# Optimization experiments

Hardware: AMD Instinct MI355X
Metric: run time of the kernel (lower is better)

The kernel has to match this reference:

```python
import jax, jax.numpy as jnp
import numpy as np

H, T, D = 16, 2048, 1024
DH = D // H  # 64


def setup_inputs() -> dict:
    key = jax.random.key(0)
    ks = jax.random.split(key, 6)
    state = jax.random.normal(ks[0], (H, DH, DH), jnp.float32) * 0.02  # per-head recurrent state
    x = jax.random.normal(ks[1], (T, D), jnp.float32)
    done = jax.random.uniform(ks[2], (T,)) < (4.0 / T)  # sparse episode-reset flags (bool)
    w_qkv = jax.random.normal(ks[3], (D, 3 * D), jnp.float32) / np.sqrt(D)
    b_qkv = jnp.zeros((3 * D,), jnp.float32)
    w_out = jax.random.normal(ks[4], (D, D), jnp.float32) / np.sqrt(D)
    b_out = jnp.zeros((D,), jnp.float32)
    return {"state": state, "x": x, "done": done, "w_qkv": w_qkv,
            "b_qkv": b_qkv, "w_out": w_out, "b_out": b_out}


def _mha_forward(state, x, done, w_qkv, b_qkv, w_out, b_out):
    # qkv projection; einops 'T (QKV H Dh) -> QKV H T Dh'
    qkv = (x @ w_qkv + b_qkv).reshape(T, 3, H, DH).transpose(1, 2, 0, 3)
    q, k, v = qkv[0], qkv[1], qkv[2]  # each (H, T, Dh)

    cum = jnp.cumsum(done.astype(jnp.int32))  # inclusive cumsum, as in done.cumsum()
    before_first = cum == 0            # tokens before first reset (attend to carried state)
    after_last = cum == cum[-1]        # tokens after last reset (feed new state)
    done_any = cum[-1] > 0

    # make_attn_mask(done): causal AND no reset index i with s < i <= t.
    # The scanned mask equals: causal & (cum[t] == cum[s]) (same-segment).
    t_idx = jnp.arange(T)
    mask = (t_idx[:, None] >= t_idx[None, :]) & (cum[:, None] == cum[None, :])  # (T, T)

    attn = jnp.where(mask[None], jnp.einsum('htd,hsd->hts', q, k), 0.0)  # mask * (q @ k.T)
    q_bef = q * before_first[None, :, None]
    out = jnp.einsum('hts,hsd->htd', attn, v) + jnp.einsum('htd,hde->hte', q_bef, state)

    k_aft = k * after_last[None, :, None]
    v_aft = v * after_last[None, :, None]
    s_new = jnp.einsum('htd,hte->hde', k_aft, v_aft)  # k_aft.T @ v_aft per head
    new_state = jnp.where(done_any, s_new, state + s_new)

    # 'H T Dh -> T (H Dh)' then output projection
    x_out = out.transpose(1, 0, 2).reshape(T, D) @ w_out + b_out
    return new_state, x_out


def reference(state, x, done, w_qkv, b_qkv, w_out, b_out):
    return _mha_forward(state, x, done, w_qkv, b_qkv, w_out, b_out)
```

## Files before the change

### kernel.cpp

```cpp
#include <hip/hip_runtime.h>

#define TT 2048
#define DD 1024
#define HH 16
#define DH 64
#define QKV_N 3072
#define QKW 2048

typedef __attribute__((ext_vector_type(8))) short bf16x8;
typedef __attribute__((ext_vector_type(4))) short short4v;
typedef __attribute__((ext_vector_type(4))) float f32x4;

__device__ inline short f2bf(float f) {
    union { float f; unsigned u; } v; v.f = f;
    unsigned r = v.u + 0x7fff + ((v.u >> 16) & 1);
    return (short)(r >> 16);
}

__device__ inline f32x4 mfma16(bf16x8 a, bf16x8 b, f32x4 c) {
    return __builtin_amdgcn_mfma_f32_16x16x32_bf16(a, b, c, 0, 0, 0);
}

__device__ __forceinline__ void gload16(const void* g, void* l) {
    __builtin_amdgcn_global_load_lds(
        (const __attribute__((address_space(1))) unsigned int*)g,
        (__attribute__((address_space(3))) unsigned int*)l, 16, 0, 0);
}

__device__ void transpose_tile(const float* __restrict__ in, short* __restrict__ out,
                               int R, int C, int r0, int c0, float (*tile)[65]) {
    int tid = threadIdx.x;
#pragma unroll
    for (int p = 0; p < 4; ++p) {
        int ch = tid + p * 256;
        int r = ch >> 4, c4 = (ch & 15) * 4;
        float4 v = *(const float4*)&in[(size_t)(r0 + r) * C + c0 + c4];
        tile[r][c4] = v.x; tile[r][c4 + 1] = v.y; tile[r][c4 + 2] = v.z; tile[r][c4 + 3] = v.w;
    }
    __syncthreads();
#pragma unroll
    for (int p = 0; p < 2; ++p) {
        int ch = tid + p * 256;
        int c = ch >> 3, r8 = (ch & 7) * 8;
        short tmp[8];
#pragma unroll
        for (int i = 0; i < 8; ++i) tmp[i] = f2bf(tile[r8 + i][c]);
        *(float4*)&out[(size_t)(c0 + c) * R + r0 + r8] = *(float4*)tmp;
    }
}

__global__ __launch_bounds__(256) void prep_kernel(const float* __restrict__ x,
                                                   const float* __restrict__ w_qkv,
                                                   const float* __restrict__ w_out,
                                                   const float* __restrict__ state,
                                                   const int* __restrict__ done,
                                                   const float* __restrict__ b_out,
                                                   short* __restrict__ x_bf,
                                                   short* __restrict__ wqT,
                                                   short* __restrict__ woT,
                                                   short* __restrict__ stT,
                                                   float* __restrict__ stout,
                                                   float* __restrict__ x_out,
                                                   int* __restrict__ seg,
                                                   int* __restrict__ totalp,
                                                   int* __restrict__ aux) {
    __shared__ float tile[64][65];
    __shared__ int scanbuf[2048 + 512 + 1];
    int b = blockIdx.x;
    int tid = threadIdx.x;
    if (b < 1024) {
        int i = (b * 256 + tid) * 8;
        float4 a = *(const float4*)&x[i];
        float4 c = *(const float4*)&x[i + 4];
        short tmp[8] = {f2bf(a.x), f2bf(a.y), f2bf(a.z), f2bf(a.w),
                        f2bf(c.x), f2bf(c.y), f2bf(c.z), f2bf(c.w)};
        *(float4*)&x_bf[i] = *(float4*)tmp;
    } else if (b < 1792) {
        int bb = b - 1024;
        transpose_tile(w_qkv, wqT, DD, QKV_N, (bb & 15) * 64, (bb >> 4) * 64, tile);
    } else if (b < 2048) {
        int bb = b - 1792;
        transpose_tile(w_out, woT, DD, DD, (bb & 15) * 64, (bb >> 4) * 64, tile);
    } else if (b < 2064) {
        int h = b - 2048;
        transpose_tile(state + (size_t)h * 4096, stT + (size_t)h * 4096, DH, DH, 0, 0, tile);
    } else if (b < 2128) {
        __shared__ int anyf;
        if (tid == 0) anyf = 0;
        __syncthreads();
        int acc = 0;
#pragma unroll
        for (int i = 0; i < 8; ++i) acc |= done[tid * 8 + i];
        if (acc) anyf = 1;
        __syncthreads();
        int f = ((b - 2064) * 256 + tid) * 4;
        float4 v = anyf ? make_float4(0.f, 0.f, 0.f, 0.f) : *(const float4*)&state[f];
        *(float4*)&stout[f] = v;
    } else if (b < 4176) {
        int f = ((b - 2128) * 256 + tid) * 4;
        int col = f & (DD - 1);
        *(float4*)&x_out[f] = *(const float4*)&b_out[col];
    } else {
        int* segl = scanbuf;
        int* part = scanbuf + 2048;
        int* excl = scanbuf + 2304;
        int base = tid * 8;
        int local[8];
        int run = 0;
#pragma unroll
        for (int i = 0; i < 8; ++i) { run += (done[base + i] != 0) ? 1 : 0; local[i] = run; }
        part[tid] = run;
        __syncthreads();
        if (tid < 64) {
            int p4[4];
#pragma unroll
            for (int i = 0; i < 4; ++i) p4[i] = part[tid * 4 + i];
            int s = p4[0] + p4[1] + p4[2] + p4[3];
            int v = s;
#pragma unroll
            for (int off = 1; off < 64; off <<= 1) {
                int u = __shfl_up(v, off);
                if (tid >= off) v += u;
            }
            int ex = v - s;
#pragma unroll
            for (int i = 0; i < 4; ++i) { excl[tid * 4 + i] = ex; ex += p4[i]; }
            if (tid == 63) { totalp[0] = v; scanbuf[2560] = v; }
        }
        __syncthreads();
        int off = excl[tid];
#pragma unroll
        for (int i = 0; i < 8; ++i) {
            int sv = off + local[i];
            seg[base + i] = sv;
            segl[base + i] = sv;
        }
        __syncthreads();
        if (tid < 33) {
            int target = (tid < 32) ? segl[tid * 64] : scanbuf[2560];
            int lo = 0, hi = 2047;
            while (lo < hi) { int mid = (lo + hi) >> 1; if (segl[mid] >= target) hi = mid; else lo = mid + 1; }
            aux[tid] = lo >> 6;
        }
    }
}

__global__ __launch_bounds__(256) void gemm_qkv(const short* __restrict__ A,
                                                const short* __restrict__ BT,
                                                const float* __restrict__ bias,
                                                short* __restrict__ qk,
                                                short* __restrict__ vt) {
    __shared__ __align__(16) short As[2][128 * 32];
    __shared__ __align__(16) short Bs[2][128 * 32];
    const int K = DD;
    int tid = threadIdx.x;
    int wave = tid >> 6, lane = tid & 63;
    int quad = lane >> 4, l15 = lane & 15;
    int m0 = blockIdx.x * 128, n0 = blockIdx.y * 128;
    int wr = (wave >> 1) * 64, wc = (wave & 1) * 64;

    int srow = wave * 32 + (lane >> 2);
    int scol = (lane & 3) * 8;
    const short* Ag = A + (size_t)(m0 + srow) * K + scol;
    const short* Bg = BT + (size_t)(n0 + srow) * K + scol;

    f32x4 acc[4][4] = {};
    for (int k0 = 0; k0 < K; k0 += 64) {
        __syncthreads();
#pragma unroll
        for (int g = 0; g < 2; ++g)
#pragma unroll
            for (int ks = 0; ks < 2; ++ks) {
                gload16(Ag + (size_t)g * 16 * K + k0 + ks * 32, &As[ks][(wave * 32 + g * 16) * 32]);
                gload16(Bg + (size_t)g * 16 * K + k0 + ks * 32, &Bs[ks][(wave * 32 + g * 16) * 32]);
            }
        __syncthreads();
#pragma unroll
        for (int ks = 0; ks < 2; ++ks) {
            bf16x8 af[4], bfr[4];
#pragma unroll
            for (int i = 0; i < 4; ++i) {
                af[i]  = *(const bf16x8*)&As[ks][(wr + i * 16 + l15) * 32 + quad * 8];
                bfr[i] = *(const bf16x8*)&Bs[ks][(wc + i * 16 + l15) * 32 + quad * 8];
            }
#pragma unroll
            for (int i = 0; i < 4; ++i)
#pragma unroll
                for (int j = 0; j < 4; ++j)
                    acc[i][j] = mfma16(af[i], bfr[j], acc[i][j]);
        }
    }

    if (n0 < 2048) {
#pragma unroll
        for (int i = 0; i < 4; ++i)
#pragma unroll
            for (int j = 0; j < 4; ++j)
#pragma unroll
                for (int r = 0; r < 4; ++r) {
                    int row = m0 + wr + i * 16 + quad * 4 + r;
                    int col = n0 + wc + j * 16 + l15;
                    qk[(size_t)row * QKW + col] = f2bf(acc[i][j][r] + bias[col]);
                }
    } else {
#pragma unroll
        for (int j = 0; j < 4; ++j) {
            int col = n0 + wc + j * 16 + l15;
            float bv = bias[col];
            int eg = col - 2048;
            int hh = eg >> 6, e = eg & 63;
#pragma unroll
            for (int i = 0; i < 4; ++i) {
                int tb = m0 + wr + i * 16 + quad * 4;
                short4v pk;
#pragma unroll
                for (int r = 0; r < 4; ++r) pk[r] = f2bf(acc[i][j][r] + bv);
                *(short4v*)&vt[(size_t)hh * (DH * TT) + (size_t)e * TT + tb] = pk;
            }
        }
    }
}

__global__ __launch_bounds__(256) void attn_mfma(const short* __restrict__ qk,
                                                 const short* __restrict__ vt,
                                                 const short* __restrict__ stT,
                                                 const int* __restrict__ seg,
                                                 const int* __restrict__ totalp,
                                                 const int* __restrict__ aux,
                                                 short* __restrict__ outb,
                                                 float* __restrict__ part,
                                                 float* __restrict__ nsout) {
    __shared__ __align__(16) short Qh[2][64 * 32];
    __shared__ __align__(16) short Kh[2][2][64 * 32];
    __shared__ __align__(16) short Vh[2][2][64 * 32];
    __shared__ __align__(16) short Ss[64 * 72];

    int h = blockIdx.x, tt = blockIdx.y, z = blockIdx.z;
    int t0 = tt * 64;
    int tid = threadIdx.x, wave = tid >> 6, lane = tid & 63;
    int quad = lane >> 4, l15 = lane & 15;
    int myt = wave * 16;
    const short* vbase = vt + (size_t)h * (DH * TT);

    if (z == 8) {
        if (tt < aux[32]) return;
        int total = totalp[0];
        int myd = wave * 16;
        short* K0 = Kh[0][0];
        short* K1 = Kh[0][1];
        bool keep = (seg[t0 + lane] == total);
        const short* src = qk + (size_t)(t0 + lane) * QKW + 1024 + h * DH + myd;
        union { float4 f; short s[8]; } u0, u1;
        u0.f = keep ? *(const float4*)src : make_float4(0.f, 0.f, 0.f, 0.f);
        u1.f = keep ? *(const float4*)(src + 8) : make_float4(0.f, 0.f, 0.f, 0.f);
        short* dst = (lane < 32) ? &K0[lane] : &K1[lane - 32];
#pragma unroll
        for (int i = 0; i < 8; ++i) {
            dst[(myd + i) * 32] = u0.s[i];
            dst[(myd + 8 + i) * 32] = u1.s[i];
        }
        bf16x8 a0 = *(const bf16x8*)&K0[(myd + l15) * 32 + quad * 8];
        bf16x8 a1 = *(const bf16x8*)&K1[(myd + l15) * 32 + quad * 8];
        f32x4 acc2[4] = {};
#pragma unroll
        for (int j = 0; j < 4; ++j) {
            const short* vrow = vbase + (size_t)(j * 16 + l15) * TT + t0 + quad * 8;
            bf16x8 b0 = *(const bf16x8*)vrow;
            bf16x8 b1 = *(const bf16x8*)(vrow + 32);
            acc2[j] = mfma16(a0, b0, acc2[j]);
            acc2[j] = mfma16(a1, b1, acc2[j]);
        }
        float* oh = nsout + (size_t)h * 4096;
#pragma unroll
        for (int j = 0; j < 4; ++j)
#pragma unroll
            for (int r = 0; r < 4; ++r)
                atomicAdd(&oh[(myd + quad * 4 + r) * DH + j * 16 + l15], acc2[j][r]);
        return;
    }

    int st0 = aux[tt];
    int sc_lo = st0 >> 2, sc_hi = tt >> 2;
    if (z < sc_lo || z > sc_hi) return;
    bool direct = (sc_lo == sc_hi);
    int st_lo = (st0 > z * 4) ? st0 : z * 4;
    int st_hi = (tt < z * 4 + 3) ? tt : z * 4 + 3;

    int sr = lane >> 2;
    int ch = lane & 3;
    const short* kg = qk + 1024 + h * DH;

    {
#pragma unroll
        for (int h2 = 0; h2 < 2; ++h2)
            gload16(qk + (size_t)(t0 + myt + sr) * QKW + h * DH + h2 * 32 + ch * 8,
                    &Qh[h2][myt * 32]);
        int s0 = st_lo * 64;
        gload16(kg + (size_t)(s0 + myt + sr) * QKW + ch * 8,      &Kh[0][0][myt * 32]);
        gload16(kg + (size_t)(s0 + myt + sr) * QKW + 32 + ch * 8, &Kh[0][1][myt * 32]);
        gload16(vbase + (size_t)(myt + sr) * TT + s0 + ch * 8,    &Vh[0][0][myt * 32]);
        gload16(vbase + (size_t)(myt + sr) * TT + s0 + 32 + ch * 8, &Vh[0][1][myt * 32]);
    }
    __syncthreads();

    bf16x8 af[2];
#pragma unroll
    for (int h2 = 0; h2 < 2; ++h2)
        af[h2] = *(const bf16x8*)&Qh[h2][(myt + l15) * 32 + quad * 8];

    int t_val = t0 + myt + l15;
    int seg_lane = seg[t_val];

    f32x4 acc2[4] = {};
    if (z == sc_lo && seg[t0] == 0) {
        const short* sb = stT + (size_t)h * 4096;
#pragma unroll
        for (int j = 0; j < 4; ++j)
#pragma unroll
            for (int h2 = 0; h2 < 2; ++h2) {
                bf16x8 a = *(const bf16x8*)(sb + (j * 16 + l15) * 64 + h2 * 32 + quad * 8);
                acc2[j] = mfma16(a, af[h2], acc2[j]);
            }
        if (seg_lane != 0) {
#pragma unroll
            for (int j = 0; j < 4; ++j)
#pragma unroll
                for (int r = 0; r < 4; ++r) acc2[j][r] = 0.f;
        }
    }

    int p = 0;
    for (int st = st_lo; st <= st_hi; ++st, p ^= 1) {
        if (st != st_lo) __syncthreads();
        if (st + 1 <= st_hi) {
            int s1 = (st + 1) * 64;
            gload16(kg + (size_t)(s1 + myt + sr) * QKW + ch * 8,        &Kh[p ^ 1][0][myt * 32]);
            gload16(kg + (size_t)(s1 + myt + sr) * QKW + 32 + ch * 8,   &Kh[p ^ 1][1][myt * 32]);
            gload16(vbase + (size_t)(myt + sr) * TT + s1 + ch * 8,      &Vh[p ^ 1][0][myt * 32]);
            gload16(vbase + (size_t)(myt + sr) * TT + s1 + 32 + ch * 8, &Vh[p ^ 1][1][myt * 32]);
        }
        int s0 = st * 64;

        f32x4 sacc[4] = {};
#pragma unroll
        for (int j = 0; j < 4; ++j)
#pragma unroll
            for (int h2 = 0; h2 < 2; ++h2) {
                bf16x8 kb = *(const bf16x8*)&Kh[p][h2][(j * 16 + l15) * 32 + quad * 8];
                sacc[j] = mfma16(kb, af[h2], sacc[j]);
            }
        int4 seg4[4];
#pragma unroll
        for (int j = 0; j < 4; ++j)
            seg4[j] = *(const int4*)&seg[s0 + j * 16 + quad * 4];
#pragma unroll
        for (int j = 0; j < 4; ++j) {
            short4v pk;
#pragma unroll
            for (int r = 0; r < 4; ++r) {
                int s_val = s0 + j * 16 + quad * 4 + r;
                int sv = (r == 0) ? seg4[j].x : (r == 1) ? seg4[j].y : (r == 2) ? seg4[j].z : seg4[j].w;
                bool ok = (sv == seg_lane) && (s_val <= t_val);
                pk[r] = ok ? f2bf(sacc[j][r]) : (short)0;
            }
            *(short4v*)&Ss[(myt + l15) * 72 + j * 16 + quad * 4] = pk;
        }
        bf16x8 sf[2];
#pragma unroll
        for (int h2 = 0; h2 < 2; ++h2)
            sf[h2] = *(const bf16x8*)&Ss[(myt + l15) * 72 + h2 * 32 + quad * 8];
#pragma unroll
        for (int j = 0; j < 4; ++j)
#pragma unroll
            for (int h2 = 0; h2 < 2; ++h2) {
                bf16x8 vb = *(const bf16x8*)&Vh[p][h2][(j * 16 + l15) * 32 + quad * 8];
                acc2[j] = mfma16(vb, sf[h2], acc2[j]);
            }
    }

    if (direct) {
#pragma unroll
        for (int j = 0; j < 4; ++j) {
            short4v pk;
#pragma unroll
            for (int r = 0; r < 4; ++r) pk[r] = f2bf(acc2[j][r]);
            *(short4v*)&outb[(size_t)t_val * DD + h * DH + j * 16 + quad * 4] = pk;
        }
    } else {
        float* pb = part + ((size_t)((h * 32 + tt) * 8 + z)) * 4096;
#pragma unroll
        for (int j = 0; j < 4; ++j)
            *(f32x4*)&pb[(myt + l15) * 64 + j * 16 + quad * 4] = acc2[j];
    }
}

__global__ __launch_bounds__(256) void attn_reduce(const float* __restrict__ part,
                                                   const int* __restrict__ aux,
                                                   short* __restrict__ outb) {
    int h = blockIdx.x, tt = blockIdx.y;
    int sc_lo = aux[tt] >> 2, sc_hi = tt >> 2;
    if (sc_lo == sc_hi) return;
    int t0 = tt * 64;
    int tid = threadIdx.x;
    const float* pb = part + ((size_t)(h * 32 + tt) * 8) * 4096;
#pragma unroll
    for (int p = 0; p < 4; ++p) {
        int idx = p * 256 + tid;
        int row = idx >> 4, c4 = (idx & 15) * 4;
        float4 acc = make_float4(0.f, 0.f, 0.f, 0.f);
        for (int sc = sc_lo; sc <= sc_hi; ++sc) {
            float4 v = *(const float4*)&pb[(size_t)sc * 4096 + row * 64 + c4];
            acc.x += v.x; acc.y += v.y; acc.z += v.z; acc.w += v.w;
        }
        short4v pk;
        pk[0] = f2bf(acc.x); pk[1] = f2bf(acc.y); pk[2] = f2bf(acc.z); pk[3] = f2bf(acc.w);
        *(short4v*)&outb[(size_t)(t0 + row) * DD + h * DH + c4] = pk;
    }
}

__global__ __launch_bounds__(256) void gemm_out(const short* __restrict__ A,
                                                const short* __restrict__ BT,
                                                float* __restrict__ Cout,
                                                int M, int N, int K) {
    __shared__ __align__(16) short As[128 * 32];
    __shared__ __align__(16) short Bs[128 * 32];
    int tid = threadIdx.x;
    int wave = tid >> 6, lane = tid & 63;
    int quad = lane >> 4, l15 = lane & 15;
    int m0 = blockIdx.x * 128, n0 = blockIdx.y * 128;
    int kb0 = blockIdx.z * (K / 2), kb1 = kb0 + K / 2;
    int wr = (wave >> 1) * 64, wc = (wave & 1) * 64;

    int srow = wave * 16 + (lane >> 2);
    int scol = (lane & 3) * 8;
    const short* Ag = A + (size_t)(m0 + srow) * K + scol;
    const short* Bg = BT + (size_t)(n0 + srow) * K + scol;
    short* As0 = &As[(wave * 16) * 32];
    short* As1 = &As[(64 + wave * 16) * 32];
    short* Bs0 = &Bs[(wave * 16) * 32];
    short* Bs1 = &Bs[(64 + wave * 16) * 32];

    f32x4 acc[4][4] = {};
    for (int k0 = kb0; k0 < kb1; k0 += 32) {
        __syncthreads();
        gload16(Ag + k0, As0);
        gload16(Ag + (size_t)64 * K + k0, As1);
        gload16(Bg + k0, Bs0);
        gload16(Bg + (size_t)64 * K + k0, Bs1);
        __syncthreads();
        bf16x8 af[4], bfr[4];
#pragma unroll
        for (int i = 0; i < 4; ++i) {
            af[i]  = *(const bf16x8*)&As[(wr + i * 16 + l15) * 32 + quad * 8];
            bfr[i] = *(const bf16x8*)&Bs[(wc + i * 16 + l15) * 32 + quad * 8];
        }
#pragma unroll
        for (int i = 0; i < 4; ++i)
#pragma unroll
            for (int j = 0; j < 4; ++j)
                acc[i][j] = mfma16(af[i], bfr[j], acc[i][j]);
    }
#pragma unroll
    for (int i = 0; i < 4; ++i)
#pragma unroll
        for (int j = 0; j < 4; ++j)
#pragma unroll
            for (int r = 0; r < 4; ++r) {
                int row = m0 + wr + i * 16 + quad * 4 + r;
                int col = n0 + wc + j * 16 + l15;
                atomicAdd(&Cout[(size_t)row * N + col], acc[i][j][r]);
            }
}

extern "C" void kernel_launch(void* const* d_in, const int* in_sizes, int n_in,
                              void* d_out, int out_size, void* d_ws, size_t ws_size,
                              hipStream_t stream) {
    const float* state = (const float*)d_in[0];
    const float* x     = (const float*)d_in[1];
    const int*   done  = (const int*)d_in[2];
    const float* w_qkv = (const float*)d_in[3];
    const float* b_qkv = (const float*)d_in[4];
    const float* w_out = (const float*)d_in[5];
    const float* b_out = (const float*)d_in[6];

    char* ws = (char*)d_ws;
    int*   seg    = (int*)ws;
    int*   totalp = (int*)(ws + 8192);
    int*   aux    = (int*)(ws + 8256);
    short* wqT    = (short*)(ws + 8448);
    short* woT    = (short*)(ws + 6299904);
    short* stT    = (short*)(ws + 8397056);
    short* qk     = (short*)(ws + 8528128);
    short* vt     = (short*)(ws + 16916736);
    short* xbf_outb = (short*)(ws + 21111040);
    float* part   = (float*)(ws + 25305344);

    float* new_state_out = (float*)d_out;
    float* x_out         = (float*)d_out + HH * DH * DH;

    prep_kernel<<<4177, 256, 0, stream>>>(x, w_qkv, w_out, state, done, b_out,
                                          xbf_outb, wqT, woT, stT,
                                          new_state_out, x_out, seg, totalp, aux);

    gemm_qkv<<<dim3(TT / 128, QKV_N / 128), 256, 0, stream>>>(
        xbf_outb, wqT, b_qkv, qk, vt);

    attn_mfma<<<dim3(HH, TT / 64, 9), 256, 0, stream>>>(
        qk, vt, stT, seg, totalp, aux, xbf_outb, part, new_state_out);

    attn_reduce<<<dim3(HH, TT / 64), 256, 0, stream>>>(part, aux, xbf_outb);

    gemm_out<<<dim3(TT / 128, DD / 128, 2), 256, 0, stream>>>(
        xbf_outb, woT, x_out, TT, DD, DD);
}
```

Baseline: 159.4 us.

## Fuse all stages into one persistent cooperative kernel with grid syncs

Replaces the five-kernel launch chain with a single cooperative persistent kernel of 512 blocks. Stages are separated by grid.sync, and the attention and state tasks are handed out through an atomic ticket queue. The QKV GEMM is retiled to 128x96 so each block owns one tile. The intent is to remove launch gaps and tail effects between stages. In exchange it adds grid-wide barrier cost and can lose occupancy or tile efficiency, and it keeps a multi-kernel fallback for when the cooperative launch fails.

New measurement: 473.0 us. 2.97x slower.

```diff
diff --git a/kernel.cpp b/kernel.cpp
--- a/kernel.cpp
+++ b/kernel.cpp
@@ -1,4 +1,5 @@
 #include <hip/hip_runtime.h>
+#include <hip/hip_cooperative_groups.h>
 
 #define TT 2048
 #define DD 1024
@@ -49,25 +50,13 @@
     }
 }
 
-__global__ __launch_bounds__(256) void prep_kernel(const float* __restrict__ x,
-                                                   const float* __restrict__ w_qkv,
-                                                   const float* __restrict__ w_out,
-                                                   const float* __restrict__ state,
-                                                   const int* __restrict__ done,
-                                                   const float* __restrict__ b_out,
-                                                   short* __restrict__ x_bf,
-                                                   short* __restrict__ wqT,
-                                                   short* __restrict__ woT,
-                                                   short* __restrict__ stT,
-                                                   float* __restrict__ stout,
-                                                   float* __restrict__ x_out,
-                                                   int* __restrict__ seg,
-                                                   int* __restrict__ totalp,
-                                                   int* __restrict__ aux) {
-    __shared__ float tile[64][65];
-    __shared__ int scanbuf[2048 + 512 + 1];
-    int b = blockIdx.x;
-    int tid = threadIdx.x;
+__device__ void prep_task(int b, int tid,
+                          const float* x, const float* w_qkv, const float* w_out,
+                          const float* state, const int* done, const float* b_out,
+                          short* x_bf, short* wqT, short* woT, short* stT,
+                          float* stout, float* x_out,
+                          int* seg, int* totalp, int* aux, int* ticket,
+                          float (*tile)[65], int* scanbuf) {
     if (b < 1024) {
         int i = (b * 256 + tid) * 8;
         float4 a = *(const float4*)&x[i];
@@ -85,14 +74,18 @@
         int h = b - 2048;
         transpose_tile(state + (size_t)h * 4096, stT + (size_t)h * 4096, DH, DH, 0, 0, tile);
     } else if (b < 2128) {
-        __shared__ int anyf;
-        if (tid == 0) anyf = 0;
-        __syncthreads();
         int acc = 0;
 #pragma unroll
         for (int i = 0; i < 8; ++i) acc |= done[tid * 8 + i];
-        if (acc) anyf = 1;
-        __syncthreads();
+        scanbuf[tid] = acc;
+        __syncthreads();
+        int any = 0;
+        for (int i = 0; i < 4; ++i) any |= scanbuf[((tid >> 2) * 4 + i) & 255];
+        any = __ballot(any != 0) != 0ull ? 1 : 0;
+        __syncthreads();
+        if (tid == 0) scanbuf[256] = any;
+        __syncthreads();
+        int anyf = scanbuf[256];
         int f = ((b - 2064) * 256 + tid) * 4;
         float4 v = anyf ? make_float4(0.f, 0.f, 0.f, 0.f) : *(const float4*)&state[f];
         *(float4*)&stout[f] = v;
@@ -102,19 +95,20 @@
         *(float4*)&x_out[f] = *(const float4*)&b_out[col];
     } else {
         int* segl = scanbuf;
-        int* part = scanbuf + 2048;
+        int* partb = scanbuf + 2048;
         int* excl = scanbuf + 2304;
         int base = tid * 8;
         int local[8];
         int run = 0;
 #pragma unroll
         for (int i = 0; i < 8; ++i) { run += (done[base + i] != 0) ? 1 : 0; local[i] = run; }
-        part[tid] = run;
+        partb[tid] = run;
+        if (tid == 0) *ticket = 0;
         __syncthreads();
         if (tid < 64) {
             int p4[4];
 #pragma unroll
-            for (int i = 0; i < 4; ++i) p4[i] = part[tid * 4 + i];
+            for (int i = 0; i < 4; ++i) p4[i] = partb[tid * 4 + i];
             int s = p4[0] + p4[1] + p4[2] + p4[3];
             int v = s;
 #pragma unroll
@@ -145,11 +139,381 @@
     }
 }
 
-__global__ __launch_bounds__(256) void gemm_qkv(const short* __restrict__ A,
-                                                const short* __restrict__ BT,
-                                                const float* __restrict__ bias,
-                                                short* __restrict__ qk,
-                                                short* __restrict__ vt) {
+__device__ void attn_task(int h, int tt, int z,
+                          const short* qk, const short* vt, const short* stT,
+                          const int* seg, const int* aux,
+                          short* outb, float* part,
+                          short* Qh0, short* Qh1, short* KhB, short* VhB, short* Ss,
+                          int tid, int wave, int lane, int quad, int l15) {
+    int st0 = aux[tt];
+    int sc_lo = st0 >> 2, sc_hi = tt >> 2;
+    if (z < sc_lo || z > sc_hi) return;
+    bool direct = (sc_lo == sc_hi);
+    int st_lo = (st0 > z * 4) ? st0 : z * 4;
+    int st_hi = (tt < z * 4 + 3) ? tt : z * 4 + 3;
+
+    int t0 = tt * 64;
+    int myt = wave * 16;
+    int sr = lane >> 2, ch = lane & 3;
+    const short* vbase = vt + (size_t)h * (DH * TT);
+    const short* kg = qk + 1024 + h * DH;
+
+    {
+        gload16(qk + (size_t)(t0 + myt + sr) * QKW + h * DH + ch * 8, Qh0 + myt * 32);
+        gload16(qk + (size_t)(t0 + myt + sr) * QKW + h * DH + 32 + ch * 8, Qh1 + myt * 32);
+        int s0 = st_lo * 64;
+        gload16(kg + (size_t)(s0 + myt + sr) * QKW + ch * 8,        KhB + 0 * 2048 + myt * 32);
+        gload16(kg + (size_t)(s0 + myt + sr) * QKW + 32 + ch * 8,   KhB + 1 * 2048 + myt * 32);
+        gload16(vbase + (size_t)(myt + sr) * TT + s0 + ch * 8,      VhB + 0 * 2048 + myt * 32);
+        gload16(vbase + (size_t)(myt + sr) * TT + s0 + 32 + ch * 8, VhB + 1 * 2048 + myt * 32);
+    }
+    __syncthreads();
+
+    bf16x8 af0 = *(const bf16x8*)&Qh0[(myt + l15) * 32 + quad * 8];
+    bf16x8 af1 = *(const bf16x8*)&Qh1[(myt + l15) * 32 + quad * 8];
+    int t_val = t0 + myt + l15;
+    int seg_lane = seg[t_val];
+
+    f32x4 acc2[4] = {};
+    if (z == sc_lo && seg[t0] == 0) {
+        const short* sb = stT + (size_t)h * 4096;
+#pragma unroll
+        for (int j = 0; j < 4; ++j) {
+            bf16x8 a0 = *(const bf16x8*)(sb + (j * 16 + l15) * 64 + quad * 8);
+            bf16x8 a1 = *(const bf16x8*)(sb + (j * 16 + l15) * 64 + 32 + quad * 8);
+            acc2[j] = mfma16(a0, af0, acc2[j]);
+            acc2[j] = mfma16(a1, af1, acc2[j]);
+        }
+        if (seg_lane != 0) {
+#pragma unroll
+            for (int j = 0; j < 4; ++j)
+#pragma unroll
+                for (int r = 0; r < 4; ++r) acc2[j][r] = 0.f;
+        }
+    }
+
+    int p = 0;
+    for (int st = st_lo; st <= st_hi; ++st, p ^= 1) {
+        if (st != st_lo) __syncthreads();
+        if (st + 1 <= st_hi) {
+            int s1 = (st + 1) * 64;
+            gload16(kg + (size_t)(s1 + myt + sr) * QKW + ch * 8,        KhB + ((p ^ 1) * 2 + 0) * 2048 + myt * 32);
+            gload16(kg + (size_t)(s1 + myt + sr) * QKW + 32 + ch * 8,   KhB + ((p ^ 1) * 2 + 1) * 2048 + myt * 32);
+            gload16(vbase + (size_t)(myt + sr) * TT + s1 + ch * 8,      VhB + ((p ^ 1) * 2 + 0) * 2048 + myt * 32);
+            gload16(vbase + (size_t)(myt + sr) * TT + s1 + 32 + ch * 8, VhB + ((p ^ 1) * 2 + 1) * 2048 + myt * 32);
+        }
+        int s0 = st * 64;
+
+        f32x4 sacc[4] = {};
+#pragma unroll
+        for (int j = 0; j < 4; ++j) {
+            bf16x8 kb0 = *(const bf16x8*)&KhB[(p * 2 + 0) * 2048 + (j * 16 + l15) * 32 + quad * 8];
+            bf16x8 kb1 = *(const bf16x8*)&KhB[(p * 2 + 1) * 2048 + (j * 16 + l15) * 32 + quad * 8];
+            sacc[j] = mfma16(kb0, af0, sacc[j]);
+            sacc[j] = mfma16(kb1, af1, sacc[j]);
+        }
+        int4 seg4[4];
+#pragma unroll
+        for (int j = 0; j < 4; ++j)
+            seg4[j] = *(const int4*)&seg[s0 + j * 16 + quad * 4];
+#pragma unroll
+        for (int j = 0; j < 4; ++j) {
+            short4v pk;
+#pragma unroll
+            for (int r = 0; r < 4; ++r) {
+                int s_val = s0 + j * 16 + quad * 4 + r;
+                int sv = (r == 0) ? seg4[j].x : (r == 1) ? seg4[j].y : (r == 2) ? seg4[j].z : seg4[j].w;
+                bool ok = (sv == seg_lane) && (s_val <= t_val);
+                pk[r] = ok ? f2bf(sacc[j][r]) : (short)0;
+            }
+            *(short4v*)&Ss[(myt + l15) * 72 + j * 16 + quad * 4] = pk;
+        }
+        bf16x8 sf0 = *(const bf16x8*)&Ss[(myt + l15) * 72 + quad * 8];
+        bf16x8 sf1 = *(const bf16x8*)&Ss[(myt + l15) * 72 + 32 + quad * 8];
+#pragma unroll
+        for (int j = 0; j < 4; ++j) {
+            bf16x8 vb0 = *(const bf16x8*)&VhB[(p * 2 + 0) * 2048 + (j * 16 + l15) * 32 + quad * 8];
+            bf16x8 vb1 = *(const bf16x8*)&VhB[(p * 2 + 1) * 2048 + (j * 16 + l15) * 32 + quad * 8];
+            acc2[j] = mfma16(vb0, sf0, acc2[j]);
+            acc2[j] = mfma16(vb1, sf1, acc2[j]);
+        }
+    }
+
+    if (direct) {
+#pragma unroll
+        for (int j = 0; j < 4; ++j) {
+            short4v pk;
+#pragma unroll
+            for (int r = 0; r < 4; ++r) pk[r] = f2bf(acc2[j][r]);
+            *(short4v*)&outb[(size_t)t_val * DD + h * DH + j * 16 + quad * 4] = pk;
+        }
+    } else {
+        float* pb = part + ((size_t)((h * 32 + tt) * 8 + z)) * 4096;
+#pragma unroll
+        for (int j = 0; j < 4; ++j)
+            *(f32x4*)&pb[(myt + l15) * 64 + j * 16 + quad * 4] = acc2[j];
+    }
+}
+
+__device__ void state_task(int h, int ct, const short* qk, const short* vt,
+                           const int* seg, int total, float* nsout,
+                           short* K0, short* K1,
+                           int wave, int lane, int quad, int l15) {
+    int t0 = ct * 64;
+    int myd = wave * 16;
+    const short* vbase = vt + (size_t)h * (DH * TT);
+    bool keep = (seg[t0 + lane] == total);
+    const short* src = qk + (size_t)(t0 + lane) * QKW + 1024 + h * DH + myd;
+    union { float4 f; short s[8]; } u0, u1;
+    u0.f = keep ? *(const float4*)src : make_float4(0.f, 0.f, 0.f, 0.f);
+    u1.f = keep ? *(const float4*)(src + 8) : make_float4(0.f, 0.f, 0.f, 0.f);
+    short* dst = (lane < 32) ? &K0[lane] : &K1[lane - 32];
+#pragma unroll
+    for (int i = 0; i < 8; ++i) {
+        dst[(myd + i) * 32] = u0.s[i];
+        dst[(myd + 8 + i) * 32] = u1.s[i];
+    }
+    bf16x8 a0 = *(const bf16x8*)&K0[(myd + l15) * 32 + quad * 8];
+    bf16x8 a1 = *(const bf16x8*)&K1[(myd + l15) * 32 + quad * 8];
+    f32x4 acc2[4] = {};
+#pragma unroll
+    for (int j = 0; j < 4; ++j) {
+        const short* vrow = vbase + (size_t)(j * 16 + l15) * TT + t0 + quad * 8;
+        bf16x8 b0 = *(const bf16x8*)vrow;
+        bf16x8 b1 = *(const bf16x8*)(vrow + 32);
+        acc2[j] = mfma16(a0, b0, acc2[j]);
+        acc2[j] = mfma16(a1, b1, acc2[j]);
+    }
+    float* oh = nsout + (size_t)h * 4096;
+#pragma unroll
+    for (int j = 0; j < 4; ++j)
+#pragma unroll
+        for (int r = 0; r < 4; ++r)
+            atomicAdd(&oh[(myd + quad * 4 + r) * DH + j * 16 + l15], acc2[j][r]);
+}
+
+__global__ __launch_bounds__(256, 2) void mega_kernel(
+    const float* __restrict__ x, const float* __restrict__ w_qkv,
+    const float* __restrict__ w_out, const float* __restrict__ state,
+    const int* __restrict__ done, const float* __restrict__ b_qkv,
+    const float* __restrict__ b_out, char* __restrict__ ws,
+    float* __restrict__ dout) {
+    __shared__ __align__(16) char smem[50192];
+    cooperative_groups::grid_group grid = cooperative_groups::this_grid();
+
+    int* seg    = (int*)ws;
+    int* totalp = (int*)(ws + 8192);
+    int* ticket = (int*)(ws + 8200);
+    int* aux    = (int*)(ws + 8256);
+    short* wqT  = (short*)(ws + 8448);
+    short* woT  = (short*)(ws + 6299904);
+    short* stT  = (short*)(ws + 8397056);
+    short* qk   = (short*)(ws + 8528128);
+    short* vt   = (short*)(ws + 16916736);
+    short* xbf  = (short*)(ws + 21111040);
+    float* part = (float*)(ws + 25305344);
+    float* nsout = dout;
+    float* x_out = dout + HH * DH * DH;
+
+    int tid = threadIdx.x, wave = tid >> 6, lane = tid & 63;
+    int quad = lane >> 4, l15 = lane & 15;
+
+    {
+        float (*tile)[65] = (float(*)[65])smem;
+        int* scanbuf = (int*)(smem + 16640);
+        for (int t = blockIdx.x; t < 4177; t += gridDim.x) {
+            __syncthreads();
+            prep_task(t, tid, x, w_qkv, w_out, state, done, b_out,
+                      xbf, wqT, woT, stT, nsout, x_out, seg, totalp, aux, ticket,
+                      tile, scanbuf);
+        }
+    }
+    grid.sync();
+
+    {
+        short* As = (short*)smem;
+        short* Bs = (short*)(smem + 8192);
+        int m0 = (blockIdx.x & 15) * 128, n0 = (blockIdx.x >> 4) * 96;
+        int sr = lane >> 2, scol = (lane & 3) * 8;
+        const short* Ag = xbf + (size_t)(m0 + wave * 32 + sr) * DD + scol;
+        int wr = (wave >> 1) * 64, wc = (wave & 1) * 48;
+
+        f32x4 acc[4][3] = {};
+        for (int k0 = 0; k0 < DD; k0 += 32) {
+            __syncthreads();
+            gload16(Ag + k0, &As[(wave * 32) * 32]);
+            gload16(Ag + (size_t)16 * DD + k0, &As[(wave * 32 + 16) * 32]);
+            if (wave < 2) {
+                const short* Bg = wqT + (size_t)(n0 + wave * 32 + sr) * DD + scol;
+                gload16(Bg + k0, &Bs[(wave * 32) * 32]);
+                gload16(Bg + (size_t)16 * DD + k0, &Bs[(wave * 32 + 16) * 32]);
+            } else {
+                const short* Bg = wqT + (size_t)(n0 + 64 + (wave - 2) * 16 + sr) * DD + scol;
+                gload16(Bg + k0, &Bs[(64 + (wave - 2) * 16) * 32]);
+            }
+            __syncthreads();
+            bf16x8 af[4], bfr[3];
+#pragma unroll
+            for (int i = 0; i < 4; ++i)
+                af[i] = *(const bf16x8*)&As[(wr + i * 16 + l15) * 32 + quad * 8];
+#pragma unroll
+            for (int j = 0; j < 3; ++j)
+                bfr[j] = *(const bf16x8*)&Bs[(wc + j * 16 + l15) * 32 + quad * 8];
+#pragma unroll
+            for (int i = 0; i < 4; ++i)
+#pragma unroll
+                for (int j = 0; j < 3; ++j)
+                    acc[i][j] = mfma16(af[i], bfr[j], acc[i][j]);
+        }
+#pragma unroll
+        for (int j = 0; j < 3; ++j) {
+            int colbase = n0 + wc + j * 16;
+            int col = colbase + l15;
+            float bv = b_qkv[col];
+            if (colbase < 2048) {
+#pragma unroll
+                for (int i = 0; i < 4; ++i)
+#pragma unroll
+                    for (int r = 0; r < 4; ++r) {
+                        int row = m0 + wr + i * 16 + quad * 4 + r;
+                        qk[(size_t)row * QKW + col] = f2bf(acc[i][j][r] + bv);
+                    }
+            } else {
+                int eg = col - 2048;
+                int hh = eg >> 6, e = eg & 63;
+#pragma unroll
+                for (int i = 0; i < 4; ++i) {
+                    int tb = m0 + wr + i * 16 + quad * 4;
+                    short4v pk;
+#pragma unroll
+                    for (int r = 0; r < 4; ++r) pk[r] = f2bf(acc[i][j][r] + bv);
+                    *(short4v*)&vt[(size_t)hh * (DH * TT) + (size_t)e * TT + tb] = pk;
+                }
+            }
+        }
+    }
+    grid.sync();
+
+    {
+        short* Qh0 = (short*)smem;
+        short* Qh1 = Qh0 + 64 * 32;
+        short* KhB = (short*)(smem + 8192);
+        short* VhB = (short*)(smem + 24576);
+        short* Ss  = (short*)(smem + 40960);
+        int* tix   = (int*)(smem + 50176);
+        int aux32 = aux[32];
+        int total = totalp[0];
+        short* outb = xbf;
+        while (true) {
+            __syncthreads();
+            if (tid == 0) *tix = atomicAdd(ticket, 1);
+            __syncthreads();
+            int tk = *tix;
+            if (tk >= 2816) break;
+            if (tk < 2304) {
+                int h = tk & 15, idx = tk >> 4;
+                int g = 0;
+                while (g < 7 && idx >= 2 * (g + 1) * (g + 2)) ++g;
+                int rem = idx - 2 * g * (g + 1);
+                int k = rem / (g + 1), z = rem % (g + 1);
+                int tt = 4 * g + k;
+                attn_task(h, tt, z, qk, vt, stT, seg, aux, outb, part,
+                          Qh0, Qh1, KhB, VhB, Ss, tid, wave, lane, quad, l15);
+            } else {
+                int sid = tk - 2304;
+                int h = sid & 15, ct = sid >> 4;
+                if (ct < aux32) continue;
+                state_task(h, ct, qk, vt, seg, total, nsout,
+                           KhB, KhB + 2048, wave, lane, quad, l15);
+            }
+        }
+    }
+    grid.sync();
+
+    {
+        int h = blockIdx.x & 15, tt = blockIdx.x >> 4;
+        int sc_lo = aux[tt] >> 2, sc_hi = tt >> 2;
+        if (sc_lo != sc_hi) {
+            short* outb = xbf;
+            int t0 = tt * 64;
+            const float* pb = part + ((size_t)(h * 32 + tt) * 8) * 4096;
+#pragma unroll
+            for (int p = 0; p < 4; ++p) {
+                int idx = p * 256 + tid;
+                int row = idx >> 4, c4 = (idx & 15) * 4;
+                float4 acc = make_float4(0.f, 0.f, 0.f, 0.f);
+                for (int sc = sc_lo; sc <= sc_hi; ++sc) {
+                    float4 v = *(const float4*)&pb[(size_t)sc * 4096 + row * 64 + c4];
+                    acc.x += v.x; acc.y += v.y; acc.z += v.z; acc.w += v.w;
+                }
+                short4v pk;
+                pk[0] = f2bf(acc.x); pk[1] = f2bf(acc.y); pk[2] = f2bf(acc.z); pk[3] = f2bf(acc.w);
+                *(short4v*)&outb[(size_t)(t0 + row) * DD + h * DH + c4] = pk;
+            }
+        }
+    }
+    grid.sync();
+
+    {
+        short* As = (short*)smem;
+        short* Bs = (short*)(smem + 8192);
+        const short* outb = xbf;
+        int m0 = (blockIdx.x & 15) * 128;
+        int n0 = ((blockIdx.x >> 4) & 15) * 64;
+        int kz = blockIdx.x >> 8;
+        int sr = lane >> 2, scol = (lane & 3) * 8;
+        const short* Ag = outb + (size_t)(m0 + wave * 32 + sr) * DD + scol;
+        const short* Bg = woT + (size_t)(n0 + wave * 16 + sr) * DD + scol;
+        int wr = wave * 32;
+
+        f32x4 acc[2][4] = {};
+        for (int k0 = kz * 512; k0 < kz * 512 + 512; k0 += 32) {
+            __syncthreads();
+            gload16(Ag + k0, &As[(wave * 32) * 32]);
+            gload16(Ag + (size_t)16 * DD + k0, &As[(wave * 32 + 16) * 32]);
+            gload16(Bg + k0, &Bs[(wave * 16) * 32]);
+            __syncthreads();
+            bf16x8 af[2], bfr[4];
+#pragma unroll
+            for (int i = 0; i < 2; ++i)
+                af[i] = *(const bf16x8*)&As[(wr + i * 16 + l15) * 32 + quad * 8];
+#pragma unroll
+            for (int j = 0; j < 4; ++j)
+                bfr[j] = *(const bf16x8*)&Bs[(j * 16 + l15) * 32 + quad * 8];
+#pragma unroll
+            for (int i = 0; i < 2; ++i)
+#pragma unroll
+                for (int j = 0; j < 4; ++j)
+                    acc[i][j] = mfma16(af[i], bfr[j], acc[i][j]);
+        }
+#pragma unroll
+        for (int i = 0; i < 2; ++i)
+#pragma unroll
+            for (int j = 0; j < 4; ++j)
+#pragma unroll
+                for (int r = 0; r < 4; ++r) {
+                    int row = m0 + wr + i * 16 + quad * 4 + r;
+                    int col = n0 + j * 16 + l15;
+                    atomicAdd(&x_out[(size_t)row * DD + col], acc[i][j][r]);
+                }
+    }
+}
+
+__global__ __launch_bounds__(256) void fb_prep(const float* x, const float* w_qkv,
+                                               const float* w_out, const float* state,
+                                               const int* done, const float* b_out,
+                                               short* x_bf, short* wqT, short* woT,
+                                               short* stT, float* stout, float* x_out,
+                                               int* seg, int* totalp, int* aux, int* ticket) {
+    __shared__ __align__(16) char smem[27140];
+    float (*tile)[65] = (float(*)[65])smem;
+    int* scanbuf = (int*)(smem + 16640);
+    prep_task(blockIdx.x, threadIdx.x, x, w_qkv, w_out, state, done, b_out,
+              x_bf, wqT, woT, stT, stout, x_out, seg, totalp, aux, ticket, tile, scanbuf);
+}
+
+__global__ __launch_bounds__(256) void fb_gemm_qkv(const short* A, const short* BT,
+                                                   const float* bias, short* qk, short* vt) {
     __shared__ __align__(16) short As[2][128 * 32];
     __shared__ __align__(16) short Bs[2][128 * 32];
     const int K = DD;
@@ -158,7 +522,6 @@
     int quad = lane >> 4, l15 = lane & 15;
     int m0 = blockIdx.x * 128, n0 = blockIdx.y * 128;
     int wr = (wave >> 1) * 64, wc = (wave & 1) * 64;
-
     int srow = wave * 32 + (lane >> 2);
     int scol = (lane & 3) * 8;
     const short* Ag = A + (size_t)(m0 + srow) * K + scol;
@@ -190,7 +553,6 @@
                     acc[i][j] = mfma16(af[i], bfr[j], acc[i][j]);
         }
     }
-
     if (n0 < 2048) {
 #pragma unroll
         for (int i = 0; i < 4; ++i)
@@ -221,182 +583,31 @@
     }
 }
 
-__global__ __launch_bounds__(256) void attn_mfma(const short* __restrict__ qk,
-                                                 const short* __restrict__ vt,
-                                                 const short* __restrict__ stT,
-                                                 const int* __restrict__ seg,
-                                                 const int* __restrict__ totalp,
-                                                 const int* __restrict__ aux,
-                                                 short* __restrict__ outb,
-                                                 float* __restrict__ part,
-                                                 float* __restrict__ nsout) {
-    __shared__ __align__(16) short Qh[2][64 * 32];
-    __shared__ __align__(16) short Kh[2][2][64 * 32];
-    __shared__ __align__(16) short Vh[2][2][64 * 32];
-    __shared__ __align__(16) short Ss[64 * 72];
-
-    int h = blockIdx.x, tt = blockIdx.y, z = blockIdx.z;
-    int t0 = tt * 64;
+__global__ __launch_bounds__(256) void fb_attn(const short* qk, const short* vt,
+                                               const short* stT, const int* seg,
+                                               const int* totalp, const int* aux,
+                                               short* outb, float* part, float* nsout) {
+    __shared__ __align__(16) char smem[50176];
+    short* Qh0 = (short*)smem;
+    short* Qh1 = Qh0 + 64 * 32;
+    short* KhB = (short*)(smem + 8192);
+    short* VhB = (short*)(smem + 24576);
+    short* Ss  = (short*)(smem + 40960);
     int tid = threadIdx.x, wave = tid >> 6, lane = tid & 63;
     int quad = lane >> 4, l15 = lane & 15;
-    int myt = wave * 16;
-    const short* vbase = vt + (size_t)h * (DH * TT);
-
+    int h = blockIdx.x, tt = blockIdx.y, z = blockIdx.z;
     if (z == 8) {
         if (tt < aux[32]) return;
-        int total = totalp[0];
-        int myd = wave * 16;
-        short* K0 = Kh[0][0];
-        short* K1 = Kh[0][1];
-        bool keep = (seg[t0 + lane] == total);
-        const short* src = qk + (size_t)(t0 + lane) * QKW + 1024 + h * DH + myd;
-        union { float4 f; short s[8]; } u0, u1;
-        u0.f = keep ? *(const float4*)src : make_float4(0.f, 0.f, 0.f, 0.f);
-        u1.f = keep ? *(const float4*)(src + 8) : make_float4(0.f, 0.f, 0.f, 0.f);
-        short* dst = (lane < 32) ? &K0[lane] : &K1[lane - 32];
-#pragma unroll
-        for (int i = 0; i < 8; ++i) {
-            dst[(myd + i) * 32] = u0.s[i];
-            dst[(myd + 8 + i) * 32] = u1.s[i];
-        }
-        bf16x8 a0 = *(const bf16x8*)&K0[(myd + l15) * 32 + quad * 8];
-        bf16x8 a1 = *(const bf16x8*)&K1[(myd + l15) * 32 + quad * 8];
-        f32x4 acc2[4] = {};
-#pragma unroll
-        for (int j = 0; j < 4; ++j) {
-            const short* vrow = vbase + (size_t)(j * 16 + l15) * TT + t0 + quad * 8;
-            bf16x8 b0 = *(const bf16x8*)vrow;
-            bf16x8 b1 = *(const bf16x8*)(vrow + 32);
-            acc2[j] = mfma16(a0, b0, acc2[j]);
-            acc2[j] = mfma16(a1, b1, acc2[j]);
-        }
-        float* oh = nsout + (size_t)h * 4096;
-#pragma unroll
-        for (int j = 0; j < 4; ++j)
-#pragma unroll
-            for (int r = 0; r < 4; ++r)
-                atomicAdd(&oh[(myd + quad * 4 + r) * DH + j * 16 + l15], acc2[j][r]);
+        state_task(h, tt, qk, vt, seg, totalp[0], nsout, KhB, KhB + 2048,
+                   wave, lane, quad, l15);
         return;
     }
-
-    int st0 = aux[tt];
-    int sc_lo = st0 >> 2, sc_hi = tt >> 2;
-    if (z < sc_lo || z > sc_hi) return;
-    bool direct = (sc_lo == sc_hi);
-    int st_lo = (st0 > z * 4) ? st0 : z * 4;
-    int st_hi = (tt < z * 4 + 3) ? tt : z * 4 + 3;
-
-    int sr = lane >> 2;
-    int ch = lane & 3;
-    const short* kg = qk + 1024 + h * DH;
-
-    {
-#pragma unroll
-        for (int h2 = 0; h2 < 2; ++h2)
-            gload16(qk + (size_t)(t0 + myt + sr) * QKW + h * DH + h2 * 32 + ch * 8,
-                    &Qh[h2][myt * 32]);
-        int s0 = st_lo * 64;
-        gload16(kg + (size_t)(s0 + myt + sr) * QKW + ch * 8,      &Kh[0][0][myt * 32]);
-        gload16(kg + (size_t)(s0 + myt + sr) * QKW + 32 + ch * 8, &Kh[0][1][myt * 32]);
-        gload16(vbase + (size_t)(myt + sr) * TT + s0 + ch * 8,    &Vh[0][0][myt * 32]);
-        gload16(vbase + (size_t)(myt + sr) * TT + s0 + 32 + ch * 8, &Vh[0][1][myt * 32]);
-    }
-    __syncthreads();
-
-    bf16x8 af[2];
-#pragma unroll
-    for (int h2 = 0; h2 < 2; ++h2)
-        af[h2] = *(const bf16x8*)&Qh[h2][(myt + l15) * 32 + quad * 8];
-
-    int t_val = t0 + myt + l15;
-    int seg_lane = seg[t_val];
-
-    f32x4 acc2[4] = {};
-    if (z == sc_lo && seg[t0] == 0) {
-        const short* sb = stT + (size_t)h * 4096;
-#pragma unroll
-        for (int j = 0; j < 4; ++j)
-#pragma unroll
-            for (int h2 = 0; h2 < 2; ++h2) {
-                bf16x8 a = *(const bf16x8*)(sb + (j * 16 + l15) * 64 + h2 * 32 + quad * 8);
-                acc2[j] = mfma16(a, af[h2], acc2[j]);
-            }
-        if (seg_lane != 0) {
-#pragma unroll
-            for (int j = 0; j < 4; ++j)
-#pragma unroll
-                for (int r = 0; r < 4; ++r) acc2[j][r] = 0.f;
-        }
-    }
-
-    int p = 0;
-    for (int st = st_lo; st <= st_hi; ++st, p ^= 1) {
-        if (st != st_lo) __syncthreads();
-        if (st + 1 <= st_hi) {
-            int s1 = (st + 1) * 64;
-            gload16(kg + (size_t)(s1 + myt + sr) * QKW + ch * 8,        &Kh[p ^ 1][0][myt * 32]);
-            gload16(kg + (size_t)(s1 + myt + sr) * QKW + 32 + ch * 8,   &Kh[p ^ 1][1][myt * 32]);
-            gload16(vbase + (size_t)(myt + sr) * TT + s1 + ch * 8,      &Vh[p ^ 1][0][myt * 32]);
-            gload16(vbase + (size_t)(myt + sr) * TT + s1 + 32 + ch * 8, &Vh[p ^ 1][1][myt * 32]);
-        }
-        int s0 = st * 64;
-
-        f32x4 sacc[4] = {};
-#pragma unroll
-        for (int j = 0; j < 4; ++j)
-#pragma unroll
-            for (int h2 = 0; h2 < 2; ++h2) {
-                bf16x8 kb = *(const bf16x8*)&Kh[p][h2][(j * 16 + l15) * 32 + quad * 8];
-                sacc[j] = mfma16(kb, af[h2], sacc[j]);
-            }
-        int4 seg4[4];
-#pragma unroll
-        for (int j = 0; j < 4; ++j)
-            seg4[j] = *(const int4*)&seg[s0 + j * 16 + quad * 4];
-#pragma unroll
-        for (int j = 0; j < 4; ++j) {
-            short4v pk;
-#pragma unroll
-            for (int r = 0; r < 4; ++r) {
-                int s_val = s0 + j * 16 + quad * 4 + r;
-                int sv = (r == 0) ? seg4[j].x : (r == 1) ? seg4[j].y : (r == 2) ? seg4[j].z : seg4[j].w;
-                bool ok = (sv == seg_lane) && (s_val <= t_val);
-                pk[r] = ok ? f2bf(sacc[j][r]) : (short)0;
-            }
-            *(short4v*)&Ss[(myt + l15) * 72 + j * 16 + quad * 4] = pk;
-        }
-        bf16x8 sf[2];
-#pragma unroll
-        for (int h2 = 0; h2 < 2; ++h2)
-            sf[h2] = *(const bf16x8*)&Ss[(myt + l15) * 72 + h2 * 32 + quad * 8];
-#pragma unroll
-        for (int j = 0; j < 4; ++j)
-#pragma unroll
-            for (int h2 = 0; h2 < 2; ++h2) {
-                bf16x8 vb = *(const bf16x8*)&Vh[p][h2][(j * 16 + l15) * 32 + quad * 8];
-                acc2[j] = mfma16(vb, sf[h2], acc2[j]);
-            }
-    }
-
-    if (direct) {
-#pragma unroll
-        for (int j = 0; j < 4; ++j) {
-            short4v pk;
-#pragma unroll
-            for (int r = 0; r < 4; ++r) pk[r] = f2bf(acc2[j][r]);
-            *(short4v*)&outb[(size_t)t_val * DD + h * DH + j * 16 + quad * 4] = pk;
-        }
-    } else {
-        float* pb = part + ((size_t)((h * 32 + tt) * 8 + z)) * 4096;
-#pragma unroll
-        for (int j = 0; j < 4; ++j)
-            *(f32x4*)&pb[(myt + l15) * 64 + j * 16 + quad * 4] = acc2[j];
-    }
-}
-
-__global__ __launch_bounds__(256) void attn_reduce(const float* __restrict__ part,
-                                                   const int* __restrict__ aux,
-                                                   short* __restrict__ outb) {
+    attn_task(h, tt, z, qk, vt, stT, seg, aux, outb, part,
+              Qh0, Qh1, KhB, VhB, Ss, tid, wave, lane, quad, l15);
+}
+
+__global__ __launch_bounds__(256) void fb_reduce(const float* part, const int* aux,
+                                                 short* outb) {
     int h = blockIdx.x, tt = blockIdx.y;
     int sc_lo = aux[tt] >> 2, sc_hi = tt >> 2;
     if (sc_lo == sc_hi) return;
@@ -418,35 +629,29 @@
     }
 }
 
-__global__ __launch_bounds__(256) void gemm_out(const short* __restrict__ A,
-                                                const short* __restrict__ BT,
-                                                float* __restrict__ Cout,
-                                                int M, int N, int K) {
+__global__ __launch_bounds__(256) void fb_gemm_out(const short* A, const short* BT,
+                                                   float* Cout) {
     __shared__ __align__(16) short As[128 * 32];
     __shared__ __align__(16) short Bs[128 * 32];
+    const int K = DD, N = DD;
     int tid = threadIdx.x;
     int wave = tid >> 6, lane = tid & 63;
     int quad = lane >> 4, l15 = lane & 15;
     int m0 = blockIdx.x * 128, n0 = blockIdx.y * 128;
     int kb0 = blockIdx.z * (K / 2), kb1 = kb0 + K / 2;
     int wr = (wave >> 1) * 64, wc = (wave & 1) * 64;
-
     int srow = wave * 16 + (lane >> 2);
     int scol = (lane & 3) * 8;
     const short* Ag = A + (size_t)(m0 + srow) * K + scol;
     const short* Bg = BT + (size_t)(n0 + srow) * K + scol;
-    short* As0 = &As[(wave * 16) * 32];
-    short* As1 = &As[(64 + wave * 16) * 32];
-    short* Bs0 = &Bs[(wave * 16) * 32];
-    short* Bs1 = &Bs[(64 + wave * 16) * 32];
 
     f32x4 acc[4][4] = {};
     for (int k0 = kb0; k0 < kb1; k0 += 32) {
         __syncthreads();
-        gload16(Ag + k0, As0);
-        gload16(Ag + (size_t)64 * K + k0, As1);
-        gload16(Bg + k0, Bs0);
-        gload16(Bg + (size_t)64 * K + k0, Bs1);
+        gload16(Ag + k0, &As[(wave * 16) * 32]);
+        gload16(Ag + (size_t)64 * K + k0, &As[(64 + wave * 16) * 32]);
+        gload16(Bg + k0, &Bs[(wave * 16) * 32]);
+        gload16(Bg + (size_t)64 * K + k0, &Bs[(64 + wave * 16) * 32]);
         __syncthreads();
         bf16x8 af[4], bfr[4];
 #pragma unroll
@@ -475,8 +680,8 @@
 extern "C" void kernel_launch(void* const* d_in, const int* in_sizes, int n_in,
                               void* d_out, int out_size, void* d_ws, size_t ws_size,
                               hipStream_t stream) {
+    const float* x     = (const float*)d_in[1];
     const float* state = (const float*)d_in[0];
-    const float* x     = (const float*)d_in[1];
     const int*   done  = (const int*)d_in[2];
     const float* w_qkv = (const float*)d_in[3];
     const float* b_qkv = (const float*)d_in[4];
@@ -486,30 +691,35 @@
     char* ws = (char*)d_ws;
     int*   seg    = (int*)ws;
     int*   totalp = (int*)(ws + 8192);
+    int*   ticket = (int*)(ws + 8200);
     int*   aux    = (int*)(ws + 8256);
     short* wqT    = (short*)(ws + 8448);
     short* woT    = (short*)(ws + 6299904);
     short* stT    = (short*)(ws + 8397056);
     short* qk     = (short*)(ws + 8528128);
     short* vt     = (short*)(ws + 16916736);
-    short* xbf_outb = (short*)(ws + 21111040);
+    short* xbf    = (short*)(ws + 21111040);
     float* part   = (float*)(ws + 25305344);
 
-    float* new_state_out = (float*)d_out;
-    float* x_out         = (float*)d_out + HH * DH * DH;
-
-    prep_kernel<<<4177, 256, 0, stream>>>(x, w_qkv, w_out, state, done, b_out,
-                                          xbf_outb, wqT, woT, stT,
-                                          new_state_out, x_out, seg, totalp, aux);
-
-    gemm_qkv<<<dim3(TT / 128, QKV_N / 128), 256, 0, stream>>>(
-        xbf_outb, wqT, b_qkv, qk, vt);
-
-    attn_mfma<<<dim3(HH, TT / 64, 9), 256, 0, stream>>>(
-        qk, vt, stT, seg, totalp, aux, xbf_outb, part, new_state_out);
-
-    attn_reduce<<<dim3(HH, TT / 64), 256, 0, stream>>>(part, aux, xbf_outb);
-
-    gemm_out<<<dim3(TT / 128, DD / 128, 2), 256, 0, stream>>>(
-        xbf_outb, woT, x_out, TT, DD, DD);
-}
+    float* dout = (float*)d_out;
+    float* new_state_out = dout;
+    float* x_out = dout + HH * DH * DH;
+
+    void* args[9] = {(void*)&x, (void*)&w_qkv, (void*)&w_out, (void*)&state,
+                     (void*)&done, (void*)&b_qkv, (void*)&b_out, (void*)&ws,
+                     (void*)&dout};
+    hipError_t e = hipLaunchCooperativeKernel((const void*)mega_kernel,
+                                              dim3(512), dim3(256), args, 0, stream);
+    if (e == hipSuccess) return;
+    (void)hipGetLastError();
+
+    fb_prep<<<4177, 256, 0, stream>>>(x, w_qkv, w_out, state, done, b_out,
+                                      xbf, wqT, woT, stT, new_state_out, x_out,
+                                      seg, totalp, aux, ticket);
+    fb_gemm_qkv<<<dim3(TT / 128, QKV_N / 128), 256, 0, stream>>>(
+        xbf, wqT, b_qkv, qk, vt);
+    fb_attn<<<dim3(HH, TT / 64, 9), 256, 0, stream>>>(
+        qk, vt, stT, seg, totalp, aux, xbf, part, new_state_out);
+    fb_reduce<<<dim3(HH, TT / 64), 256, 0, stream>>>(part, aux, xbf);
+    fb_gemm_out<<<dim3(TT / 128, DD / 128, 2), 256, 0, stream>>>(xbf, woT, x_out);
+}
```

## Retile QKV GEMM to 128x96 blocks with single-stage K=32 loads

Applied to the files above, without the earlier changes.

Changes the QKV projection GEMM tile from 128x128 to 128x96, so the grid grows from 384 to 512 blocks and fills the GPU's compute units more evenly. The K loop now loads 32-wide slices per iteration instead of 64-wide, which halves the LDS footprint but doubles the number of barriers. The epilogue decides per 16-column fragment whether the output goes to the qk or the transposed v layout, because a 96-wide tile can cross the 2048 boundary. Accumulator registers drop from 16 to 12 fragments per wave, in exchange for less reuse per LDS load.

New measurement: 159.8 us. Within noise of the previous version (+0.3%).

```diff
diff --git a/kernel.cpp b/kernel.cpp
--- a/kernel.cpp
+++ b/kernel.cpp
@@ -150,63 +150,61 @@
                                                 const float* __restrict__ bias,
                                                 short* __restrict__ qk,
                                                 short* __restrict__ vt) {
-    __shared__ __align__(16) short As[2][128 * 32];
-    __shared__ __align__(16) short Bs[2][128 * 32];
+    __shared__ __align__(16) short As[128 * 32];
+    __shared__ __align__(16) short Bs[96 * 32];
     const int K = DD;
     int tid = threadIdx.x;
     int wave = tid >> 6, lane = tid & 63;
     int quad = lane >> 4, l15 = lane & 15;
-    int m0 = blockIdx.x * 128, n0 = blockIdx.y * 128;
-    int wr = (wave >> 1) * 64, wc = (wave & 1) * 64;
-
-    int srow = wave * 32 + (lane >> 2);
+    int m0 = blockIdx.x * 128, n0 = blockIdx.y * 96;
+    int wr = (wave >> 1) * 64, wc = (wave & 1) * 48;
+
+    int sr = lane >> 2;
     int scol = (lane & 3) * 8;
-    const short* Ag = A + (size_t)(m0 + srow) * K + scol;
-    const short* Bg = BT + (size_t)(n0 + srow) * K + scol;
-
-    f32x4 acc[4][4] = {};
-    for (int k0 = 0; k0 < K; k0 += 64) {
-        __syncthreads();
-#pragma unroll
-        for (int g = 0; g < 2; ++g)
-#pragma unroll
-            for (int ks = 0; ks < 2; ++ks) {
-                gload16(Ag + (size_t)g * 16 * K + k0 + ks * 32, &As[ks][(wave * 32 + g * 16) * 32]);
-                gload16(Bg + (size_t)g * 16 * K + k0 + ks * 32, &Bs[ks][(wave * 32 + g * 16) * 32]);
-            }
-        __syncthreads();
-#pragma unroll
-        for (int ks = 0; ks < 2; ++ks) {
-            bf16x8 af[4], bfr[4];
-#pragma unroll
-            for (int i = 0; i < 4; ++i) {
-                af[i]  = *(const bf16x8*)&As[ks][(wr + i * 16 + l15) * 32 + quad * 8];
-                bfr[i] = *(const bf16x8*)&Bs[ks][(wc + i * 16 + l15) * 32 + quad * 8];
-            }
+    const short* Ag = A + (size_t)(m0 + wave * 32 + sr) * K + scol;
+
+    f32x4 acc[4][3] = {};
+    for (int k0 = 0; k0 < K; k0 += 32) {
+        __syncthreads();
+        gload16(Ag + k0, &As[(wave * 32) * 32]);
+        gload16(Ag + (size_t)16 * K + k0, &As[(wave * 32 + 16) * 32]);
+        if (wave < 2) {
+            const short* Bg = BT + (size_t)(n0 + wave * 32 + sr) * K + scol;
+            gload16(Bg + k0, &Bs[(wave * 32) * 32]);
+            gload16(Bg + (size_t)16 * K + k0, &Bs[(wave * 32 + 16) * 32]);
+        } else {
+            const short* Bg = BT + (size_t)(n0 + 64 + (wave - 2) * 16 + sr) * K + scol;
+            gload16(Bg + k0, &Bs[(64 + (wave - 2) * 16) * 32]);
+        }
+        __syncthreads();
+        bf16x8 af[4], bfr[3];
+#pragma unroll
+        for (int i = 0; i < 4; ++i)
+            af[i] = *(const bf16x8*)&As[(wr + i * 16 + l15) * 32 + quad * 8];
+#pragma unroll
+        for (int j = 0; j < 3; ++j)
+            bfr[j] = *(const bf16x8*)&Bs[(wc + j * 16 + l15) * 32 + quad * 8];
+#pragma unroll
+        for (int i = 0; i < 4; ++i)
+#pragma unroll
+            for (int j = 0; j < 3; ++j)
+                acc[i][j] = mfma16(af[i], bfr[j], acc[i][j]);
+    }
+
+#pragma unroll
+    for (int j = 0; j < 3; ++j) {
+        int colbase = n0 + wc + j * 16;
+        int col = colbase + l15;
+        float bv = bias[col];
+        if (colbase < 2048) {
 #pragma unroll
             for (int i = 0; i < 4; ++i)
-#pragma unroll
-                for (int j = 0; j < 4; ++j)
-                    acc[i][j] = mfma16(af[i], bfr[j], acc[i][j]);
-        }
-    }
-
-    if (n0 < 2048) {
-#pragma unroll
-        for (int i = 0; i < 4; ++i)
-#pragma unroll
-            for (int j = 0; j < 4; ++j)
 #pragma unroll
                 for (int r = 0; r < 4; ++r) {
                     int row = m0 + wr + i * 16 + quad * 4 + r;
-                    int col = n0 + wc + j * 16 + l15;
-                    qk[(size_t)row * QKW + col] = f2bf(acc[i][j][r] + bias[col]);
+                    qk[(size_t)row * QKW + col] = f2bf(acc[i][j][r] + bv);
                 }
-    } else {
-#pragma unroll
-        for (int j = 0; j < 4; ++j) {
-            int col = n0 + wc + j * 16 + l15;
-            float bv = bias[col];
+        } else {
             int eg = col - 2048;
             int hh = eg >> 6, e = eg & 63;
 #pragma unroll
@@ -502,7 +500,7 @@
                                           xbf_outb, wqT, woT, stT,
                                           new_state_out, x_out, seg, totalp, aux);
 
-    gemm_qkv<<<dim3(TT / 128, QKV_N / 128), 256, 0, stream>>>(
+    gemm_qkv<<<dim3(TT / 128, QKV_N / 96), 256, 0, stream>>>(
         xbf_outb, wqT, b_qkv, qk, vt);
 
     attn_mfma<<<dim3(HH, TT / 64, 9), 256, 0, stream>>>(
```
